# Optimization experiments

Measured on AMD Instinct MI355X. Metric: run time of the kernel, lower is better.

## Reference

```python
import jax, jax.numpy as jnp
import numpy as np

N, E, D, H = 8192, 8, 2048, 2048


def setup_inputs() -> dict:
    key = jax.random.key(0)
    k1, k2, k3, k4 = jax.random.split(key, 4)
    x = jax.random.normal(k1, (N, D), dtype=jnp.float32)
    indices = jax.random.randint(k2, (N, 1), 0, E)  # top_k=1 expert assignment
    W = jax.random.normal(k3, (E, D, H), dtype=jnp.float32) * 0.02
    b = jax.random.normal(k4, (E, H), dtype=jnp.float32) * 0.02
    return {"x": x, "indices": indices, "W": W, "b": b}


def reference(x, indices, W, b):
    # Each token is routed to exactly one expert (top_k=1):
    # expert_id[n] = indices[n, 0]. The torch module loops experts e=0..E-1,
    # gathers tokens with (indices == e).any(-1) (ascending order via nonzero),
    # applies expert e's Linear + ReLU, and concatenates outputs in expert order.
    expert_id = indices[:, 0]                              # [N]
    # Dense dispatch: compute every expert's linear on every token, then pick
    # each token's own expert row (jit-friendly; no data-dependent shapes).
    y_all = jnp.einsum('nd,edh->neh', x, W) + b[None, :, :]  # [N, E, H]
    y = jnp.take_along_axis(y_all, expert_id[:, None, None], axis=1)[:, 1 - 1, :]  # [N, H]
    y = jax.nn.relu(y)
    # Concat in expert order == stable sort of tokens by expert id
    # (nonzero returns ascending indices, so within-expert order is preserved).
    order = jnp.argsort(expert_id)  # stable by default
    return y[order]
```

## Files before the change

### kernel.cpp

```cpp
#include <hip/hip_runtime.h>

#define N_TOK 8192
#define N_EXP 8
#define DIM   2048
#define HID   2048

typedef __attribute__((ext_vector_type(8))) short short8;
typedef __attribute__((ext_vector_type(4))) float f32x4;
typedef __attribute__((ext_vector_type(4))) unsigned short ushort4v;

__device__ inline unsigned short f2bf(float f) {
  unsigned int u = __builtin_bit_cast(unsigned int, f);
  unsigned int r = u + 0x7FFFu + ((u >> 16) & 1u);
  return (unsigned short)(r >> 16);
}

__global__ __launch_bounds__(256) void sort_experts(const int* __restrict__ idx,
                                                    int* __restrict__ perm,
                                                    int* __restrict__ offs,
                                                    int* __restrict__ jobs) {
  __shared__ int cnt[256][8];
  __shared__ int base[8];
  const int t = threadIdx.x;
  int local[8] = {0,0,0,0,0,0,0,0};
  const int r0 = t * 32;
  for (int i = 0; i < 32; ++i) {
    int e = idx[r0 + i] & 7;
    ++local[e];
  }
#pragma unroll
  for (int e = 0; e < 8; ++e) cnt[t][e] = local[e];
  __syncthreads();
  if (t < 8) {
    int s = 0;
    for (int i = 0; i < 256; ++i) { int v = cnt[i][t]; cnt[i][t] = s; s += v; }
    base[t] = s;
  }
  __syncthreads();
  if (t == 0) {
    int s = 0, njm = 0;
    for (int e = 0; e < 8; ++e) {
      int v = base[e];
      offs[e] = s; base[e] = s; s += v;
      int nm = (v + 255) >> 8;
      for (int mt = 0; mt < nm; ++mt) jobs[1 + njm++] = e | (mt << 8);
    }
    offs[8] = s;
    jobs[0] = njm;
  }
  __syncthreads();
  int pos[8];
#pragma unroll
  for (int e = 0; e < 8; ++e) pos[e] = base[e] + cnt[t][e];
  for (int i = 0; i < 32; ++i) {
    int r = r0 + i;
    int e = idx[r] & 7;
    perm[pos[e]++] = r;
  }
}

__global__ __launch_bounds__(256) void prep(const float* __restrict__ x,
                                            const int* __restrict__ perm,
                                            unsigned short* __restrict__ xs,
                                            const float* __restrict__ W,
                                            unsigned short* __restrict__ Wt) {
  __shared__ unsigned short tile[64][68];
  const int t = threadIdx.x;
  if (blockIdx.x < 8192) {
    int gid = blockIdx.x * 256 + t;
    int p = gid >> 8;
    int c = gid & 255;
    int src = perm[p];
    const float* sp = x + (size_t)src * DIM + c * 8;
    float4 a = *(const float4*)sp;
    float4 b = *(const float4*)(sp + 4);
    short8 o;
    o[0] = (short)f2bf(a.x); o[1] = (short)f2bf(a.y);
    o[2] = (short)f2bf(a.z); o[3] = (short)f2bf(a.w);
    o[4] = (short)f2bf(b.x); o[5] = (short)f2bf(b.y);
    o[6] = (short)f2bf(b.z); o[7] = (short)f2bf(b.w);
    *(short8*)(xs + (size_t)p * DIM + c * 8) = o;
  } else {
    const int b = blockIdx.x - 8192;
    const int e  = b >> 10;
    const int d0 = ((b >> 5) & 31) * 64;
    const int h0 = (b & 31) * 64;
    const int cr = t & 15;
    const int rr = t >> 4;
    const float* Wp = W + ((size_t)e * DIM + d0) * HID + h0;
#pragma unroll
    for (int i = 0; i < 4; ++i) {
      int d = rr + i * 16;
      float4 v = *(const float4*)(Wp + (size_t)d * HID + cr * 4);
      ushort4v o;
      o[0] = f2bf(v.x); o[1] = f2bf(v.y); o[2] = f2bf(v.z); o[3] = f2bf(v.w);
      *(ushort4v*)&tile[d][cr * 4] = o;
    }
    __syncthreads();
    unsigned short* op = Wt + ((size_t)e * HID + h0) * DIM + d0;
#pragma unroll
    for (int i = 0; i < 4; ++i) {
      int h = rr + i * 16;
      ushort4v o;
      o[0] = tile[cr * 4 + 0][h];
      o[1] = tile[cr * 4 + 1][h];
      o[2] = tile[cr * 4 + 2][h];
      o[3] = tile[cr * 4 + 3][h];
      *(ushort4v*)(op + (size_t)h * DIM + cr * 4) = o;
    }
  }
}

#define NKT 32
#define SLOT 24576

#define MM(D,A,B) D = __builtin_amdgcn_mfma_f32_16x16x32_bf16(A, B, D, 0, 0, 0)
#define GLD(SRC, DST) __builtin_amdgcn_global_load_lds( \
    (const __attribute__((address_space(1))) void*)(SRC), \
    (__attribute__((address_space(3))) void*)(DST), 16, 0, 0)
#define BAR() __builtin_amdgcn_s_barrier()
#define PRIO(x) __builtin_amdgcn_s_setprio(x)

__global__ __launch_bounds__(512, 2) void grouped_gemm(
    const unsigned short* __restrict__ xs,
    const unsigned short* __restrict__ Wt,
    const float* __restrict__ bias,
    const int* __restrict__ offs,
    const int* __restrict__ jobs,
    float* __restrict__ out) {
  __shared__ __align__(16) unsigned short sm[3 * SLOT];

  const int t    = threadIdx.x;
  const int lane = t & 63;
  const int wid  = t >> 6;
  const int wr   = wid >> 1;
  const int wc   = wid & 1;
  const int l15  = lane & 15;
  const int l4   = lane >> 4;

  const int cb0  = (l4 * 8) ^ ((l15 & 7) << 3);
  const int cb1  = cb0 ^ 32;
  const int arow = (wr * 64 + l15) * 64;
  const int brow = 16384 + (wc * 64 + l15) * 64;

  const int r0  = t >> 3;
  const int keu = ((t & 7) * 8) ^ ((r0 & 7) << 3);
  const int dA = t * 8;

  const int njm   = jobs[0];
  const int total = njm * 16;

#pragma unroll 1
  for (int idx = blockIdx.x; idx < total; idx += 256) {
    const int jm  = jobs[1 + (idx >> 4)];
    const int e   = jm & 255;
    const int mt  = jm >> 8;
    const int nx  = idx & 15;
    const int off = offs[e];
    const int cnt = offs[e + 1] - off;
    const int aBase = off + mt * 256;
    const int n0  = nx * 128;

    unsigned int pa0, pa1, pa2, pa3, pb0, pb1;
    {
      int p;
      p = aBase + 0 * 64 + r0; if (p > N_TOK - 1) p = N_TOK - 1; pa0 = (unsigned)p * 2048 + keu;
      p = aBase + 1 * 64 + r0; if (p > N_TOK - 1) p = N_TOK - 1; pa1 = (unsigned)p * 2048 + keu;
      p = aBase + 2 * 64 + r0; if (p > N_TOK - 1) p = N_TOK - 1; pa2 = (unsigned)p * 2048 + keu;
      p = aBase + 3 * 64 + r0; if (p > N_TOK - 1) p = N_TOK - 1; pa3 = (unsigned)p * 2048 + keu;
      unsigned int eW = (unsigned)e * (DIM * HID);
      pb0 = eW + (unsigned)(n0 + 0 * 64 + r0) * 2048 + keu;
      pb1 = eW + (unsigned)(n0 + 1 * 64 + r0) * 2048 + keu;
    }

#define ST_HALF1(SBASE, KOFS) do { \
    GLD(xs + pa0 + (KOFS), sm + (SBASE) + 0 * 4096 + dA); \
    GLD(xs + pa1 + (KOFS), sm + (SBASE) + 1 * 4096 + dA); \
    GLD(xs + pa2 + (KOFS), sm + (SBASE) + 2 * 4096 + dA); } while (0)
#define ST_HALF2(SBASE, KOFS) do { \
    GLD(xs + pa3 + (KOFS), sm + (SBASE) + 3 * 4096 + dA); \
    GLD(Wt + pb0 + (KOFS), sm + (SBASE) + 16384 + 0 * 4096 + dA); \
    GLD(Wt + pb1 + (KOFS), sm + (SBASE) + 16384 + 1 * 4096 + dA); } while (0)

    f32x4 acc[4][4] = {};

    ST_HALF1(0, 0);        ST_HALF2(0, 0);
    ST_HALF1(SLOT, 64);    ST_HALF2(SLOT, 64);
    asm volatile("s_waitcnt vmcnt(6)" ::: "memory");
    BAR();

    short8 fa0, fa1, fa2, fa3, fb0, fb1, fb2, fb3;
    int sl = 0;
    int s2 = 2;

#pragma unroll 1
    for (int T = 0; T < NKT; ++T) {
      const unsigned short* SP = sm + sl * SLOT;
      const int sb = s2 * SLOT;
      const int kofs = (T + 2) * 64;
      const bool st = (T < NKT - 2);

      fa0 = *(const short8*)(SP + arow + 0 * 1024 + cb0);
      fa1 = *(const short8*)(SP + arow + 1 * 1024 + cb0);
      fa2 = *(const short8*)(SP + arow + 2 * 1024 + cb0);
      fa3 = *(const short8*)(SP + arow + 3 * 1024 + cb0);
      fb0 = *(const short8*)(SP + brow + 0 * 1024 + cb0);
      fb1 = *(const short8*)(SP + brow + 1 * 1024 + cb0);
      fb2 = *(const short8*)(SP + brow + 2 * 1024 + cb0);
      fb3 = *(const short8*)(SP + brow + 3 * 1024 + cb0);
      if (st) ST_HALF1(sb, kofs);
      BAR(); PRIO(1);
      MM(acc[0][0],fa0,fb0); MM(acc[0][1],fa0,fb1); MM(acc[0][2],fa0,fb2); MM(acc[0][3],fa0,fb3);
      MM(acc[1][0],fa1,fb0); MM(acc[1][1],fa1,fb1); MM(acc[1][2],fa1,fb2); MM(acc[1][3],fa1,fb3);
      MM(acc[2][0],fa2,fb0); MM(acc[2][1],fa2,fb1); MM(acc[2][2],fa2,fb2); MM(acc[2][3],fa2,fb3);
      MM(acc[3][0],fa3,fb0); MM(acc[3][1],fa3,fb1); MM(acc[3][2],fa3,fb2); MM(acc[3][3],fa3,fb3);
      PRIO(0); BAR();

      fa0 = *(const short8*)(SP + arow + 0 * 1024 + cb1);
      fa1 = *(const short8*)(SP + arow + 1 * 1024 + cb1);
      fa2 = *(const short8*)(SP + arow + 2 * 1024 + cb1);
      fa3 = *(const short8*)(SP + arow + 3 * 1024 + cb1);
      fb0 = *(const short8*)(SP + brow + 0 * 1024 + cb1);
      fb1 = *(const short8*)(SP + brow + 1 * 1024 + cb1);
      fb2 = *(const short8*)(SP + brow + 2 * 1024 + cb1);
      fb3 = *(const short8*)(SP + brow + 3 * 1024 + cb1);
      if (st) ST_HALF2(sb, kofs);
      BAR(); PRIO(1);
      MM(acc[0][0],fa0,fb0); MM(acc[0][1],fa0,fb1); MM(acc[0][2],fa0,fb2); MM(acc[0][3],fa0,fb3);
      MM(acc[1][0],fa1,fb0); MM(acc[1][1],fa1,fb1); MM(acc[1][2],fa1,fb2); MM(acc[1][3],fa1,fb3);
      MM(acc[2][0],fa2,fb0); MM(acc[2][1],fa2,fb1); MM(acc[2][2],fa2,fb2); MM(acc[2][3],fa2,fb3);
      MM(acc[3][0],fa3,fb0); MM(acc[3][1],fa3,fb1); MM(acc[3][2],fa3,fb2); MM(acc[3][3],fa3,fb3);
      PRIO(0);
      if (T < NKT - 2)       { asm volatile("s_waitcnt vmcnt(6)" ::: "memory"); }
      else if (T == NKT - 2) { asm volatile("s_waitcnt vmcnt(0)" ::: "memory"); }
      BAR();

      sl = (sl == 2) ? 0 : sl + 1;
      s2 = (s2 == 2) ? 0 : s2 + 1;
    }

#pragma unroll
    for (int n = 0; n < 4; ++n) {
      int col = n0 + wc * 64 + n * 16 + l15;
      float bv = bias[e * HID + col];
#pragma unroll
      for (int m = 0; m < 4; ++m) {
#pragma unroll
        for (int q = 0; q < 4; ++q) {
          int r = wr * 64 + m * 16 + l4 * 4 + q;
          if (mt * 256 + r < cnt) {
            float v = acc[m][n][q] + bv;
            out[(size_t)(off + mt * 256 + r) * HID + col] = v > 0.f ? v : 0.f;
          }
        }
      }
    }
  }
#undef ST_HALF1
#undef ST_HALF2
}

extern "C" void kernel_launch(void* const* d_in, const int* in_sizes, int n_in,
                              void* d_out, int out_size, void* d_ws, size_t ws_size,
                              hipStream_t stream) {
  const float* x   = (const float*)d_in[0];
  const int*   idx = (const int*)d_in[1];
  const float* W   = (const float*)d_in[2];
  const float* b   = (const float*)d_in[3];
  float* out = (float*)d_out;

  char* ws = (char*)d_ws;
  unsigned short* xs = (unsigned short*)ws;
  unsigned short* Wt = (unsigned short*)(ws + (size_t)N_TOK * DIM * 2);
  int* perm = (int*)(ws + (size_t)N_TOK * DIM * 2 + (size_t)N_EXP * DIM * HID * 2);
  int* offs = perm + N_TOK;
  int* jobs = offs + 16;

  sort_experts<<<1, 256, 0, stream>>>(idx, perm, offs, jobs);
  prep<<<16384, 256, 0, stream>>>(x, perm, xs, W, Wt);
  grouped_gemm<<<256, 512, 0, stream>>>(xs, Wt, b, offs, jobs, out);
}
```

Before: 188.8 us.

## Schedule GEMM tiles per XCD with atomic work queues over column pairs

Replaces the static strided tile loop with a dynamic per-XCD work queue. Each XCD (blockIdx & 7) owns two fixed N-column tiles and pulls row bands through an atomic counter. The aim is to keep each XCD's weight columns resident in its own L2 and to balance uneven expert band counts dynamically. It adds an atomic and two barriers per tile, and it assumes round-robin block-to-XCD placement.

```diff
diff --git a/kernel.cpp b/kernel.cpp
--- a/kernel.cpp
+++ b/kernel.cpp
@@ -18,7 +18,8 @@
 __global__ __launch_bounds__(256) void sort_experts(const int* __restrict__ idx,
                                                     int* __restrict__ perm,
                                                     int* __restrict__ offs,
-                                                    int* __restrict__ jobs) {
+                                                    int* __restrict__ bands,
+                                                    int* __restrict__ qcnt) {
   __shared__ int cnt[256][8];
   __shared__ int base[8];
   const int t = threadIdx.x;
@@ -35,18 +36,19 @@
     int s = 0;
     for (int i = 0; i < 256; ++i) { int v = cnt[i][t]; cnt[i][t] = s; s += v; }
     base[t] = s;
+    qcnt[t] = 32;
   }
   __syncthreads();
   if (t == 0) {
-    int s = 0, njm = 0;
+    int s = 0, nb = 0;
     for (int e = 0; e < 8; ++e) {
       int v = base[e];
       offs[e] = s; base[e] = s; s += v;
       int nm = (v + 255) >> 8;
-      for (int mt = 0; mt < nm; ++mt) jobs[1 + njm++] = e | (mt << 8);
+      for (int mt = 0; mt < nm; ++mt) bands[1 + nb++] = e | (mt << 8);
     }
     offs[8] = s;
-    jobs[0] = njm;
+    bands[0] = nb;
   }
   __syncthreads();
   int pos[8];
@@ -126,9 +128,11 @@
     const unsigned short* __restrict__ Wt,
     const float* __restrict__ bias,
     const int* __restrict__ offs,
-    const int* __restrict__ jobs,
+    const int* __restrict__ bands,
+    int* __restrict__ qcnt,
     float* __restrict__ out) {
   __shared__ __align__(16) unsigned short sm[3 * SLOT];
+  __shared__ int next_i;
 
   const int t    = threadIdx.x;
   const int lane = t & 63;
@@ -137,6 +141,7 @@
   const int wc   = wid & 1;
   const int l15  = lane & 15;
   const int l4   = lane >> 4;
+  const int xcd  = blockIdx.x & 7;
 
   const int cb0  = (l4 * 8) ^ ((l15 & 7) << 3);
   const int cb1  = cb0 ^ 32;
@@ -147,15 +152,14 @@
   const int keu = ((t & 7) * 8) ^ ((r0 & 7) << 3);
   const int dA = t * 8;
 
-  const int njm   = jobs[0];
-  const int total = njm * 16;
-
-#pragma unroll 1
-  for (int idx = blockIdx.x; idx < total; idx += 256) {
-    const int jm  = jobs[1 + (idx >> 4)];
-    const int e   = jm & 255;
-    const int mt  = jm >> 8;
-    const int nx  = idx & 15;
+  const int nj = bands[0] * 2;
+
+  int i = blockIdx.x >> 3;
+  while (i < nj) {
+    const int bd  = bands[1 + (i >> 1)];
+    const int e   = bd & 255;
+    const int mt  = bd >> 8;
+    const int nx  = (xcd << 1) | (i & 1);
     const int off = offs[e];
     const int cnt = offs[e + 1] - off;
     const int aBase = off + mt * 256;
@@ -255,6 +259,11 @@
         }
       }
     }
+
+    __syncthreads();
+    if (t == 0) next_i = atomicAdd(&qcnt[xcd], 1);
+    __syncthreads();
+    i = next_i;
   }
 #undef ST_HALF1
 #undef ST_HALF2
@@ -272,11 +281,12 @@
   char* ws = (char*)d_ws;
   unsigned short* xs = (unsigned short*)ws;
   unsigned short* Wt = (unsigned short*)(ws + (size_t)N_TOK * DIM * 2);
-  int* perm = (int*)(ws + (size_t)N_TOK * DIM * 2 + (size_t)N_EXP * DIM * HID * 2);
-  int* offs = perm + N_TOK;
-  int* jobs = offs + 16;
-
-  sort_experts<<<1, 256, 0, stream>>>(idx, perm, offs, jobs);
+  int* perm  = (int*)(ws + (size_t)N_TOK * DIM * 2 + (size_t)N_EXP * DIM * HID * 2);
+  int* offs  = perm + N_TOK;
+  int* bands = offs + 16;
+  int* qcnt  = bands + 4096;
+
+  sort_experts<<<1, 256, 0, stream>>>(idx, perm, offs, bands, qcnt);
   prep<<<16384, 256, 0, stream>>>(x, perm, xs, W, Wt);
-  grouped_gemm<<<256, 512, 0, stream>>>(xs, Wt, b, offs, jobs, out);
-}
+  grouped_gemm<<<256, 512, 0, stream>>>(xs, Wt, b, offs, bands, qcnt, out);
+}
```

After: 194.1 us. +2.8%, slower.
